# Optimization experiments

Measured on AMD Instinct MI355X. Metric: run time of the kernel, lower is better.

The kernel has to match this reference:

```python
import jax, jax.numpy as jnp
import numpy as np

# ---- static config (severity=3 -> params (0.4, 1, 1)) ----
B, C, H, W = 64, 3, 224, 224
SIGMA = 0.4
MAX_DELTA = 1
ITERATIONS = 1
RADIUS = int(4.0 * SIGMA + 0.5)  # scipy/skimage default truncate=4.0 -> radius 2
_x = np.arange(-RADIUS, RADIUS + 1, dtype=np.float64)
_k = np.exp(-0.5 * (_x / SIGMA) ** 2)
KERNEL = jnp.asarray(_k / _k.sum(), dtype=jnp.float32)  # 5 taps

# swap coordinate order: y = H-1..1 (outer), x = W-1..1 (inner), repeated ITERATIONS times
_ys = np.arange(H - MAX_DELTA, MAX_DELTA - 1, -1, dtype=np.int32)
_xs = np.arange(W - MAX_DELTA, MAX_DELTA - 1, -1, dtype=np.int32)
YS = jnp.asarray(np.tile(np.repeat(_ys, _xs.size), ITERATIONS))  # [ITER*N]
XS = jnp.asarray(np.tile(np.tile(_xs, _ys.size), ITERATIONS))    # [ITER*N]
N_SWAPS = YS.shape[0]


def _gaussian_blur(img):
    """Separable Gaussian, mode='nearest' (edge pad), img [B,H,W,C] float."""
    p = jnp.pad(img, ((0, 0), (RADIUS, RADIUS), (0, 0), (0, 0)), mode='edge')
    img = sum(KERNEL[i] * p[:, i:i + H] for i in range(2 * RADIUS + 1))
    p = jnp.pad(img, ((0, 0), (0, 0), (RADIUS, RADIUS), (0, 0)), mode='edge')
    img = sum(KERNEL[i] * p[:, :, i:i + W] for i in range(2 * RADIUS + 1))
    return img


def _swap_single(img, d):
    """Sequential random pixel swaps. img [H,W,C]; d [N_SWAPS,2] in {-1,0,1}."""
    def body(im, t):
        y, x, dy, dx = t
        yp = jnp.clip(y + dy, 0, H - 1)
        xp = jnp.clip(x + dx, 0, W - 1)
        a = im[y, x]
        b = im[yp, xp]
        # set order matches original temp-swap (self-swap is identity)
        im = im.at[y, x].set(b).at[yp, xp].set(a)
        return im, None
    im, _ = jax.lax.scan(body, img, (YS, XS, d[:, 0], d[:, 1]))
    return im


def setup_inputs() -> dict:
    key = jax.random.key(0)
    k1, k2 = jax.random.split(key)
    x = jax.random.uniform(k1, (B, C, H, W), dtype=jnp.float32)
    deltas = jax.random.randint(k2, (B, N_SWAPS, 2), 0, 3, dtype=jnp.int32)
    return {"x": x, "deltas": deltas}


def reference(x, deltas):
    # tensor_to_numpy_uint8: clamp(x*255) then byte() (truncation)
    img = jnp.floor(jnp.clip(x * 255.0, 0.0, 255.0))        # [B,C,H,W], uint8 values
    img = jnp.transpose(img, (0, 2, 3, 1))                   # [B,H,W,C]
    # first blur + np.uint8 cast (truncation)
    img = jnp.floor(_gaussian_blur(img / 255.0) * 255.0)
    # sequential random pixel swaps, per image
    d = deltas - 1                                           # values in {-1,0,1}
    img = jax.vmap(_swap_single)(img, d)
    # second blur, clip, uint8 cast, then /255 back to float tensor
    img = _gaussian_blur(img / 255.0)
    img = jnp.floor(jnp.clip(img * 255.0, 0.0, 255.0)) / 255.0
    return jnp.transpose(img, (0, 3, 1, 2))                  # [B,C,H,W]
```

## Files before the change

kernel.cpp:

```cpp
#include <hip/hip_runtime.h>
#include <hip/hip_bf16.h>

#define KW0 0.91921792f
#define KW1 0.04038762f
#define KW2 3.42560e-6f

#define HH 224
#define WW 224
#define NSW 49729
#define LEAF_SLOT 676
#define LEAF_IMG 150748
#define P_STRIDE 50176

__global__ __launch_bounds__(256) void build_kernel(const int* __restrict__ deltas,
                                                    unsigned short* __restrict__ leafG) {
    const int j = blockIdx.x;
    const int b = blockIdx.y;
    const int U = j * 32;

    __shared__ __align__(16) unsigned short smA[32 * LEAF_SLOT];
    __shared__ unsigned pk[32 * 29];

    const int tid = threadIdx.x;
    const int u = U + tid;

    {
        const int2* Dbase = (const int2*)deltas + (size_t)b * NSW + (size_t)U * 223;
        for (int w = tid; w < 32 * 28; w += 256) {
            const int r = w / 28, k = w - r * 28;
            if (U + r < 223) {
                const int base = r * 223 + 8 * k;
                unsigned word = 0;
#pragma unroll
                for (int jj = 0; jj < 8; ++jj) {
                    const int i = 8 * k + jj;
                    unsigned idx = 5u;
                    if (i < 223) {
                        int2 d = Dbase[base + jj];
                        unsigned px = (unsigned)d.x, py = (unsigned)d.y;
                        if (U + r == 0) px = min(px, 1u);
                        if (i == 0) py = min(py, 1u);
                        idx = px * 4u + py;
                    }
                    word |= idx << (4 * jj);
                }
                pk[r * 29 + k] = word;
            }
        }
    }
    __syncthreads();

    if (tid < 32 && u < 223) {
        const int y = 223 - u;
        const unsigned b0r = (unsigned)(y - 1) << 8;
        const unsigned b1r = (unsigned)y << 8;
        const unsigned b2r = (unsigned)(y + 1) << 8;
        unsigned short* Lf = &smA[tid * LEAF_SLOT];
        const unsigned* pkr = &pk[tid * 29];

        unsigned w00 = b0r + 222, w01 = b0r + 223, w02 = b0r + 224;
        unsigned w10 = b1r + 222, w11 = b1r + 223, w12 = b1r + 224;
        unsigned w20 = b2r + 222, w21 = b2r + 223, w22 = b2r + 224;

        unsigned wA_ = pkr[0], wB_ = pkr[1], wC_ = pkr[2];

#define GB_STEP(KK, CA, CB, CC) {                                               \
            const int x_ = 223 - (ibase + (KK));                                \
            const unsigned wsel_ = (((KK) >> 3) == 0) ? wA_                     \
                                 : ((((KK) >> 3) == 1) ? wB_ : wC_);            \
            const unsigned idx_ = (wsel_ >> (4 * ((KK) & 7))) & 15u;            \
            const unsigned pr_ = idx_ >> 2, pc_ = idx_ & 3u;                    \
            const bool pc0_ = (pc_ == 0u), pc1_ = (pc_ == 1u);                  \
            const bool pr0_ = (pr_ == 0u), pr1_ = (pr_ == 1u);                  \
            const unsigned s0_ = pc0_ ? w0##CA : (pc1_ ? w0##CB : w0##CC);      \
            const unsigned s1_ = pc0_ ? w1##CA : (pc1_ ? w1##CB : w1##CC);      \
            const unsigned s2_ = pc0_ ? w2##CA : (pc1_ ? w2##CB : w2##CC);      \
            const unsigned v_ = pr0_ ? s0_ : (pr1_ ? s1_ : s2_);                \
            const unsigned c_ = w1##CB;                                         \
            w0##CA = idx_ == 0u  ? c_ : w0##CA;                                 \
            w0##CB = idx_ == 1u  ? c_ : w0##CB;                                 \
            w0##CC = idx_ == 2u  ? c_ : w0##CC;                                 \
            w1##CA = idx_ == 4u  ? c_ : w1##CA;                                 \
            w1##CC = idx_ == 6u  ? c_ : w1##CC;                                 \
            w2##CA = idx_ == 8u  ? c_ : w2##CA;                                 \
            w2##CB = idx_ == 9u  ? c_ : w2##CB;                                 \
            w2##CC = idx_ == 10u ? c_ : w2##CC;                                 \
            w1##CB = v_;                                                        \
            Lf[x_ + 1]   = (unsigned short)w0##CC;                              \
            Lf[x_ + 225] = (unsigned short)w1##CC;                              \
            Lf[x_ + 449] = (unsigned short)w2##CC;                              \
            w0##CC = b0r + (unsigned)(x_ - 2);                                  \
            w1##CC = b1r + (unsigned)(x_ - 2);                                  \
            w2##CC = b2r + (unsigned)(x_ - 2);                                  \
        }
#define GB_TRIPLE(K0) GB_STEP((K0), 0, 1, 2) GB_STEP((K0)+1, 2, 0, 1) GB_STEP((K0)+2, 1, 2, 0)
        for (int blk = 0; blk < 9; ++blk) {
            const int ibase = 24 * blk;
            const unsigned nA_ = pkr[min(3 * blk + 3, 27)];
            const unsigned nB_ = pkr[min(3 * blk + 4, 27)];
            const unsigned nC_ = pkr[min(3 * blk + 5, 27)];
            GB_TRIPLE(0)  GB_TRIPLE(3)  GB_TRIPLE(6)  GB_TRIPLE(9)
            GB_TRIPLE(12) GB_TRIPLE(15) GB_TRIPLE(18) GB_TRIPLE(21)
            wA_ = nA_; wB_ = nB_; wC_ = nC_;
        }
        {
            const int ibase = 216;
            GB_TRIPLE(0) GB_TRIPLE(3) GB_STEP(6, 0, 1, 2)
        }
        Lf[1] = (unsigned short)w01; Lf[225] = (unsigned short)w11; Lf[449] = (unsigned short)w21;
        Lf[0] = (unsigned short)w00; Lf[224] = (unsigned short)w10; Lf[448] = (unsigned short)w20;
#undef GB_TRIPLE
#undef GB_STEP
    }
    __syncthreads();

    const int nuT = min(32, 223 - U);
    uint2* dst = (uint2*)(leafG + (size_t)b * LEAF_IMG + (size_t)U * LEAF_SLOT);
    const uint2* srcp = (const uint2*)smA;
    for (int l = tid; l < nuT * (LEAF_SLOT / 4); l += 256) dst[l] = srcp[l];
}

__global__ __launch_bounds__(256) void chaseP_kernel(const unsigned short* __restrict__ leafG,
                                                     unsigned short* __restrict__ P) {
    const int b = blockIdx.y;
    const int base = blockIdx.x * 2048;
    const unsigned short* L = leafG + (size_t)b * LEAF_IMG;
    unsigned short* Pb = P + (size_t)b * P_STRIDE;
    const int e0 = base + (int)threadIdx.x * 8;
    if (e0 >= P_STRIDE) return;

    unsigned rv[8], cv[8]; bool done[8]; int us[8];
    const int pr0 = e0 / 224, pc0 = e0 - pr0 * 224;
    int umax = -1;
#pragma unroll
    for (int t = 0; t < 8; ++t) {
        const int pc = pc0 + t;
        const int pr = pr0 + (pc >= 224 ? 1 : 0);
        rv[t] = (unsigned)pr;
        cv[t] = (unsigned)(pc >= 224 ? pc - 224 : pc);
        us[t] = min(222, 224 - pr);
        done[t] = false;
        umax = max(umax, us[t]);
    }
    for (int u = umax; u >= 0; --u) {
        const unsigned short* Lu = L + u * LEAF_SLOT;
        const int bot = 222 - u;
        bool all = true;
#pragma unroll
        for (int t = 0; t < 8; ++t) {
            if (!done[t] && u <= us[t]) {
                if ((int)rv[t] < bot) done[t] = true;
                else {
                    const unsigned q = Lu[__mul24((int)rv[t] - bot, 224) + (int)cv[t]];
                    rv[t] = q >> 8;
                    cv[t] = q & 255u;
                }
            }
            all = all && done[t];
        }
        if (all) break;
    }
    unsigned res[8];
#pragma unroll
    for (int t = 0; t < 8; ++t)
        res[t] = (unsigned)(__mul24((int)rv[t], 224) + (int)cv[t]);
    uint4 v;
    v.x = res[0] | (res[1] << 16);
    v.y = res[2] | (res[3] << 16);
    v.z = res[4] | (res[5] << 16);
    v.w = res[6] | (res[7] << 16);
    *(uint4*)(Pb + e0) = v;
}

__global__ __launch_bounds__(256) void blur1_kernel(const float* __restrict__ x,
                                                    unsigned char* __restrict__ img) {
    const int rb = blockIdx.x, c = blockIdx.y, b = blockIdx.z;
    const int y0 = rb * 8;
    __shared__ float A[12][WW];
    __shared__ float Bv[8][WW];
    const float* xp = x + ((size_t)(b * 3 + c)) * HH * WW;

    for (int l = threadIdx.x; l < 12 * 56; l += 256) {
        int r = l / 56, k4 = (l - r * 56) * 4;
        int gy = min(max(y0 + r - 2, 0), HH - 1);
        float4 v = *(const float4*)(xp + gy * WW + k4);
        A[r][k4]     = floorf(fminf(fmaxf(v.x * 255.0f, 0.0f), 255.0f));
        A[r][k4 + 1] = floorf(fminf(fmaxf(v.y * 255.0f, 0.0f), 255.0f));
        A[r][k4 + 2] = floorf(fminf(fmaxf(v.z * 255.0f, 0.0f), 255.0f));
        A[r][k4 + 3] = floorf(fminf(fmaxf(v.w * 255.0f, 0.0f), 255.0f));
    }
    __syncthreads();
    for (int l = threadIdx.x; l < 8 * WW; l += 256) {
        int r = l / WW, xx = l - r * WW;
        Bv[r][xx] = KW2 * A[r][xx] + KW1 * A[r + 1][xx] + KW0 * A[r + 2][xx]
                  + KW1 * A[r + 3][xx] + KW2 * A[r + 4][xx];
    }
    __syncthreads();
    unsigned char* op = img + ((size_t)(b * 3 + c)) * HH * WW;
    for (int l = threadIdx.x; l < 8 * WW; l += 256) {
        int r = l / WW, xx = l - r * WW;
        int c0 = max(xx - 2, 0), c1 = max(xx - 1, 0);
        int c3 = min(xx + 1, WW - 1), c4 = min(xx + 2, WW - 1);
        float s = KW2 * Bv[r][c0] + KW1 * Bv[r][c1] + KW0 * Bv[r][xx]
                + KW1 * Bv[r][c3] + KW2 * Bv[r][c4];
        op[(y0 + r) * WW + xx] = (unsigned char)floorf(s);
    }
}

__global__ __launch_bounds__(256) void blur2_apply_kernel(const unsigned char* __restrict__ img,
                                                          const unsigned short* __restrict__ P,
                                                          float* __restrict__ out) {
    const int rb = blockIdx.x, c = blockIdx.y, b = blockIdx.z;
    const int y0 = rb * 8;
    __shared__ float A[12][WW];
    __shared__ float Bv[8][WW];
    const unsigned char* ip = img + ((size_t)(b * 3 + c)) * HH * WW;
    const unsigned short* Pp = P + (size_t)b * P_STRIDE;

    for (int l = threadIdx.x; l < 12 * 28; l += 256) {
        int r = l / 28, g8 = (l - r * 28) * 8;
        int gy = min(max(y0 + r - 2, 0), HH - 1);
        uint4 pe = *(const uint4*)(Pp + gy * WW + g8);
        A[r][g8]     = (float)ip[pe.x & 0xffffu];
        A[r][g8 + 1] = (float)ip[pe.x >> 16];
        A[r][g8 + 2] = (float)ip[pe.y & 0xffffu];
        A[r][g8 + 3] = (float)ip[pe.y >> 16];
        A[r][g8 + 4] = (float)ip[pe.z & 0xffffu];
        A[r][g8 + 5] = (float)ip[pe.z >> 16];
        A[r][g8 + 6] = (float)ip[pe.w & 0xffffu];
        A[r][g8 + 7] = (float)ip[pe.w >> 16];
    }
    __syncthreads();
    for (int l = threadIdx.x; l < 8 * WW; l += 256) {
        int r = l / WW, xx = l - r * WW;
        Bv[r][xx] = KW2 * A[r][xx] + KW1 * A[r + 1][xx] + KW0 * A[r + 2][xx]
                  + KW1 * A[r + 3][xx] + KW2 * A[r + 4][xx];
    }
    __syncthreads();
    float* op = out + ((size_t)(b * 3 + c)) * HH * WW;
    for (int l = threadIdx.x; l < 8 * WW; l += 256) {
        int r = l / WW, xx = l - r * WW;
        int c0 = max(xx - 2, 0), c1 = max(xx - 1, 0);
        int c3 = min(xx + 1, WW - 1), c4 = min(xx + 2, WW - 1);
        float s = KW2 * Bv[r][c0] + KW1 * Bv[r][c1] + KW0 * Bv[r][xx]
                + KW1 * Bv[r][c3] + KW2 * Bv[r][c4];
        s = fminf(fmaxf(s, 0.0f), 255.0f);
        op[(y0 + r) * WW + xx] = floorf(s) / 255.0f;
    }
}

__global__ __launch_bounds__(256) void apply_kernel(unsigned char* __restrict__ img,
                                                    const unsigned short* __restrict__ P) {
    const int plane = blockIdx.x;
    const int b = plane / 3;
    __shared__ __align__(16) unsigned char im[HH * WW];
    unsigned char* g = img + (size_t)plane * (HH * WW);
    for (int l = threadIdx.x; l < (HH * WW) / 16; l += 256)
        ((int4*)im)[l] = ((const int4*)g)[l];
    __syncthreads();
    const unsigned short* Pp = P + (size_t)b * P_STRIDE;
    for (int t = threadIdx.x; t < (HH * WW) / 8; t += 256) {
        uint4 pe = ((const uint4*)Pp)[t];
        unsigned e0 = pe.x & 0xffffu, e1 = pe.x >> 16;
        unsigned e2 = pe.y & 0xffffu, e3 = pe.y >> 16;
        unsigned e4 = pe.z & 0xffffu, e5 = pe.z >> 16;
        unsigned e6 = pe.w & 0xffffu, e7 = pe.w >> 16;
        unsigned lo = (unsigned)im[e0] | ((unsigned)im[e1] << 8)
                    | ((unsigned)im[e2] << 16) | ((unsigned)im[e3] << 24);
        unsigned hi = (unsigned)im[e4] | ((unsigned)im[e5] << 8)
                    | ((unsigned)im[e6] << 16) | ((unsigned)im[e7] << 24);
        ((uint2*)g)[t] = make_uint2(lo, hi);
    }
}

__global__ __launch_bounds__(256) void blur2_kernel(const unsigned char* __restrict__ img,
                                                    float* __restrict__ out) {
    const int rb = blockIdx.x, c = blockIdx.y, b = blockIdx.z;
    const int y0 = rb * 8;
    __shared__ float A[12][WW];
    __shared__ float Bv[8][WW];
    const unsigned char* ip = img + ((size_t)(b * 3 + c)) * HH * WW;

    for (int l = threadIdx.x; l < 12 * WW; l += 256) {
        int r = l / WW, xx = l - r * WW;
        int gy = min(max(y0 + r - 2, 0), HH - 1);
        A[r][xx] = (float)ip[gy * WW + xx];
    }
    __syncthreads();
    for (int l = threadIdx.x; l < 8 * WW; l += 256) {
        int r = l / WW, xx = l - r * WW;
        Bv[r][xx] = KW2 * A[r][xx] + KW1 * A[r + 1][xx] + KW0 * A[r + 2][xx]
                  + KW1 * A[r + 3][xx] + KW2 * A[r + 4][xx];
    }
    __syncthreads();
    float* op = out + ((size_t)(b * 3 + c)) * HH * WW;
    for (int l = threadIdx.x; l < 8 * WW; l += 256) {
        int r = l / WW, xx = l - r * WW;
        int c0 = max(xx - 2, 0), c1 = max(xx - 1, 0);
        int c3 = min(xx + 1, WW - 1), c4 = min(xx + 2, WW - 1);
        float s = KW2 * Bv[r][c0] + KW1 * Bv[r][c1] + KW0 * Bv[r][xx]
                + KW1 * Bv[r][c3] + KW2 * Bv[r][c4];
        s = fminf(fmaxf(s, 0.0f), 255.0f);
        op[(y0 + r) * WW + xx] = floorf(s) / 255.0f;
    }
}

extern "C" void kernel_launch(void* const* d_in, const int* in_sizes, int n_in,
                              void* d_out, int out_size, void* d_ws, size_t ws_size,
                              hipStream_t stream) {
    const float* x      = (const float*)d_in[0];
    const int*   deltas = (const int*)d_in[1];
    float*       out    = (float*)d_out;
    unsigned char* img  = (unsigned char*)d_ws;

    const size_t imgBytes  = 9633792;
    const size_t leafBytes = (size_t)64 * LEAF_IMG * 2;
    const size_t pBytes    = (size_t)64 * P_STRIDE * 2;
    const bool big_ws = ws_size >= imgBytes + leafBytes + pBytes;

    if (big_ws) {
        unsigned short* leafG = (unsigned short*)(img + imgBytes);
        unsigned short* P     = (unsigned short*)(img + imgBytes + leafBytes);
        build_kernel<<<dim3(7, 64), 256, 0, stream>>>(deltas, leafG);
        chaseP_kernel<<<dim3(25, 64), 256, 0, stream>>>(leafG, P);
        blur1_kernel<<<dim3(28, 3, 64), 256, 0, stream>>>(x, img);
        blur2_apply_kernel<<<dim3(28, 3, 64), 256, 0, stream>>>(img, P, out);
    } else {
        unsigned short* leafG = (unsigned short*)d_out;
        unsigned short* pF    = leafG + (size_t)64 * LEAF_IMG;
        build_kernel<<<dim3(7, 64), 256, 0, stream>>>(deltas, leafG);
        chaseP_kernel<<<dim3(25, 64), 256, 0, stream>>>(leafG, pF);
        blur1_kernel<<<dim3(28, 3, 64), 256, 0, stream>>>(x, img);
        apply_kernel<<<dim3(192), 256, 0, stream>>>(img, pF);
        blur2_kernel<<<dim3(28, 3, 64), 256, 0, stream>>>(img, out);
    }
}
```

Baseline: 109.9 us.

## Fuse leaf build with pointer chase in shared memory, merge blur1 with delta packing

Merges the first blur and the delta packing into one launch, using a block-index split so the two independent jobs share one grid. Replaces the separate build and chase kernels with a single kernel per image half. That kernel builds the swap leaves in shared memory in three row chunks and chases the permutation through them, so the leaf table never round-trips through global memory. The cost is fewer kernel launches and less global traffic. In exchange, the build/chase stage runs on only 128 large blocks, and each chunk's build runs serially on up to 75 threads, which could limit parallelism.

```diff
diff --git a/kernel.cpp b/kernel.cpp
--- a/kernel.cpp
+++ b/kernel.cpp
@@ -8,64 +8,141 @@
 #define HH 224
 #define WW 224
 #define NSW 49729
-#define LEAF_SLOT 676
-#define LEAF_IMG 150748
 #define P_STRIDE 50176
-
-__global__ __launch_bounds__(256) void build_kernel(const int* __restrict__ deltas,
-                                                    unsigned short* __restrict__ leafG) {
-    const int j = blockIdx.x;
-    const int b = blockIdx.y;
-    const int U = j * 32;
-
-    __shared__ __align__(16) unsigned short smA[32 * LEAF_SLOT];
-    __shared__ unsigned pk[32 * 29];
-
+#define LSLOT 672
+
+__global__ __launch_bounds__(256) void prep2_kernel(const float* __restrict__ x,
+                                                    const int* __restrict__ deltas,
+                                                    unsigned char* __restrict__ img,
+                                                    unsigned* __restrict__ pkG) {
+    const int bid = blockIdx.x;
     const int tid = threadIdx.x;
-    const int u = U + tid;
-
-    {
-        const int2* Dbase = (const int2*)deltas + (size_t)b * NSW + (size_t)U * 223;
-        for (int w = tid; w < 32 * 28; w += 256) {
-            const int r = w / 28, k = w - r * 28;
-            if (U + r < 223) {
-                const int base = r * 223 + 8 * k;
-                unsigned word = 0;
+    __shared__ float A[12][WW];
+    __shared__ float Bv[8][WW];
+
+    if (bid < 5376) {
+        const int rb = bid % 28;
+        const int c  = (bid / 28) % 3;
+        const int b  = bid / 84;
+        const int y0 = rb * 8;
+        const float* xp = x + ((size_t)(b * 3 + c)) * HH * WW;
+
+        for (int l = tid; l < 12 * 56; l += 256) {
+            int r = l / 56, k4 = (l - r * 56) * 4;
+            int gy = min(max(y0 + r - 2, 0), HH - 1);
+            float4 v = *(const float4*)(xp + gy * WW + k4);
+            A[r][k4]     = floorf(fminf(fmaxf(v.x * 255.0f, 0.0f), 255.0f));
+            A[r][k4 + 1] = floorf(fminf(fmaxf(v.y * 255.0f, 0.0f), 255.0f));
+            A[r][k4 + 2] = floorf(fminf(fmaxf(v.z * 255.0f, 0.0f), 255.0f));
+            A[r][k4 + 3] = floorf(fminf(fmaxf(v.w * 255.0f, 0.0f), 255.0f));
+        }
+        __syncthreads();
+        for (int l = tid; l < 8 * WW; l += 256) {
+            int r = l / WW, xx = l - r * WW;
+            Bv[r][xx] = KW2 * A[r][xx] + KW1 * A[r + 1][xx] + KW0 * A[r + 2][xx]
+                      + KW1 * A[r + 3][xx] + KW2 * A[r + 4][xx];
+        }
+        __syncthreads();
+        unsigned char* op = img + ((size_t)(b * 3 + c)) * HH * WW;
+        for (int l = tid; l < 8 * WW; l += 256) {
+            int r = l / WW, xx = l - r * WW;
+            int c0 = max(xx - 2, 0), c1 = max(xx - 1, 0);
+            int c3 = min(xx + 1, WW - 1), c4 = min(xx + 2, WW - 1);
+            float s = KW2 * Bv[r][c0] + KW1 * Bv[r][c1] + KW0 * Bv[r][xx]
+                    + KW1 * Bv[r][c3] + KW2 * Bv[r][c4];
+            op[(y0 + r) * WW + xx] = (unsigned char)floorf(s);
+        }
+    } else {
+        const int pidx = (bid - 5376) * 256 + tid;
+        for (int w = pidx; w < 64 * 223 * 29; w += 448 * 256) {
+            const int word = w % 29;
+            const int rowg = w / 29;
+            const int b = rowg / 223, u = rowg - b * 223;
+            const int2* D = (const int2*)deltas + (size_t)b * NSW + (size_t)u * 223;
+            unsigned wordv;
+            if (word < 28) {
+                wordv = 0;
 #pragma unroll
                 for (int jj = 0; jj < 8; ++jj) {
-                    const int i = 8 * k + jj;
+                    const int i = 8 * word + 1 + jj;
                     unsigned idx = 5u;
                     if (i < 223) {
-                        int2 d = Dbase[base + jj];
+                        int2 d = D[i];
                         unsigned px = (unsigned)d.x, py = (unsigned)d.y;
-                        if (U + r == 0) px = min(px, 1u);
-                        if (i == 0) py = min(py, 1u);
+                        if (u == 0) px = min(px, 1u);
                         idx = px * 4u + py;
                     }
-                    word |= idx << (4 * jj);
-                }
-                pk[r * 29 + k] = word;
-            }
-        }
-    }
-    __syncthreads();
-
-    if (tid < 32 && u < 223) {
-        const int y = 223 - u;
-        const unsigned b0r = (unsigned)(y - 1) << 8;
-        const unsigned b1r = (unsigned)y << 8;
-        const unsigned b2r = (unsigned)(y + 1) << 8;
-        unsigned short* Lf = &smA[tid * LEAF_SLOT];
-        const unsigned* pkr = &pk[tid * 29];
-
-        unsigned w00 = b0r + 222, w01 = b0r + 223, w02 = b0r + 224;
-        unsigned w10 = b1r + 222, w11 = b1r + 223, w12 = b1r + 224;
-        unsigned w20 = b2r + 222, w21 = b2r + 223, w22 = b2r + 224;
-
-        unsigned wA_ = pkr[0], wB_ = pkr[1], wC_ = pkr[2];
-
+                    wordv |= idx << (4 * jj);
+                }
+            } else {
+                int2 d = D[0];
+                unsigned px = (unsigned)d.x;
+                unsigned py = min((unsigned)d.y, 1u);
+                if (u == 0) px = min(px, 1u);
+                wordv = px * 4u + py;
+            }
+            pkG[(size_t)rowg * 29 + word] = wordv;
+        }
+    }
+}
+
+__global__ __launch_bounds__(1024) void buildchase_kernel(const unsigned* __restrict__ pkG,
+                                                          unsigned short* __restrict__ P) {
+    const int sp = blockIdx.x;
+    const int b  = blockIdx.y;
+    __shared__ unsigned short leaf[75 * LSLOT];
+    __shared__ unsigned pk[75 * 29];
+    const int tid = threadIdx.x;
+    unsigned short* Pb = P + (size_t)b * P_STRIDE;
+    const unsigned* pkImg = pkG + (size_t)b * 223 * 29;
+
+    for (int ch = 0; ch < 3; ++ch) {
+        const int lo = (ch == 0) ? 148 : ((ch == 1) ? 74 : 0);
+        const int hi = (ch == 0) ? 223 : ((ch == 1) ? 148 : 74);
+        const int nr = hi - lo;
+
+        for (int w = tid; w < nr * 29; w += 1024)
+            pk[w] = pkImg[(size_t)lo * 29 + w];
+        __syncthreads();
+
+        if (tid < nr) {
+            const int u = lo + tid;
+            const int y = 223 - u;
+            const unsigned b0r = (unsigned)(y - 1) << 8;
+            const unsigned b1r = (unsigned)y << 8;
+            const unsigned b2r = (unsigned)(y + 1) << 8;
+            unsigned short* Lf = &leaf[tid * LSLOT];
+            const unsigned* pkr = &pk[tid * 29];
+
+            unsigned w00 = b0r + 222, w01 = b0r + 223, w02 = b0r + 224;
+            unsigned w10 = b1r + 222, w11 = b1r + 223, w12 = b1r + 224;
+            unsigned w20 = b2r + 222, w21 = b2r + 223, w22 = b2r + 224;
+
+            {
+                const unsigned idx_ = pkr[28] & 15u;
+                const unsigned pr_ = idx_ >> 2, pc_ = idx_ & 3u;
+                const bool pc0_ = (pc_ == 0u), pc1_ = (pc_ == 1u);
+                const bool pr0_ = (pr_ == 0u), pr1_ = (pr_ == 1u);
+                const unsigned s0_ = pc0_ ? w00 : (pc1_ ? w01 : w02);
+                const unsigned s1_ = pc0_ ? w10 : (pc1_ ? w11 : w12);
+                const unsigned s2_ = pc0_ ? w20 : (pc1_ ? w21 : w22);
+                const unsigned v_ = pr0_ ? s0_ : (pr1_ ? s1_ : s2_);
+                const unsigned c_ = w11;
+                w00 = idx_ == 0u  ? c_ : w00;
+                w01 = idx_ == 1u  ? c_ : w01;
+                w02 = idx_ == 2u  ? c_ : w02;
+                w10 = idx_ == 4u  ? c_ : w10;
+                w12 = idx_ == 6u  ? c_ : w12;
+                w20 = idx_ == 8u  ? c_ : w20;
+                w21 = idx_ == 9u  ? c_ : w21;
+                w22 = idx_ == 10u ? c_ : w22;
+                w11 = v_;
+                w02 = b0r + 221; w12 = b1r + 221; w22 = b2r + 221;
+            }
+
+            unsigned wA_ = pkr[0], wB_ = pkr[1], wC_ = pkr[2];
 #define GB_STEP(KK, CA, CB, CC) {                                               \
-            const int x_ = 223 - (ibase + (KK));                                \
+            const int x_ = 222 - (jbase + (KK));                                \
             const unsigned wsel_ = (((KK) >> 3) == 0) ? wA_                     \
                                  : ((((KK) >> 3) == 1) ? wB_ : wC_);            \
             const unsigned idx_ = (wsel_ >> (4 * ((KK) & 7))) & 15u;            \
@@ -93,117 +170,87 @@
             w1##CC = b1r + (unsigned)(x_ - 2);                                  \
             w2##CC = b2r + (unsigned)(x_ - 2);                                  \
         }
-#define GB_TRIPLE(K0) GB_STEP((K0), 0, 1, 2) GB_STEP((K0)+1, 2, 0, 1) GB_STEP((K0)+2, 1, 2, 0)
-        for (int blk = 0; blk < 9; ++blk) {
-            const int ibase = 24 * blk;
-            const unsigned nA_ = pkr[min(3 * blk + 3, 27)];
-            const unsigned nB_ = pkr[min(3 * blk + 4, 27)];
-            const unsigned nC_ = pkr[min(3 * blk + 5, 27)];
-            GB_TRIPLE(0)  GB_TRIPLE(3)  GB_TRIPLE(6)  GB_TRIPLE(9)
-            GB_TRIPLE(12) GB_TRIPLE(15) GB_TRIPLE(18) GB_TRIPLE(21)
-            wA_ = nA_; wB_ = nB_; wC_ = nC_;
-        }
-        {
-            const int ibase = 216;
-            GB_TRIPLE(0) GB_TRIPLE(3) GB_STEP(6, 0, 1, 2)
-        }
-        Lf[1] = (unsigned short)w01; Lf[225] = (unsigned short)w11; Lf[449] = (unsigned short)w21;
-        Lf[0] = (unsigned short)w00; Lf[224] = (unsigned short)w10; Lf[448] = (unsigned short)w20;
+#define GB_TRIPLE(K0) GB_STEP((K0), 2, 0, 1) GB_STEP((K0)+1, 1, 2, 0) GB_STEP((K0)+2, 0, 1, 2)
+            for (int blk = 0; blk < 9; ++blk) {
+                const int jbase = 24 * blk;
+                const unsigned nA_ = pkr[min(3 * blk + 3, 27)];
+                const unsigned nB_ = pkr[min(3 * blk + 4, 27)];
+                const unsigned nC_ = pkr[min(3 * blk + 5, 27)];
+                GB_TRIPLE(0)  GB_TRIPLE(3)  GB_TRIPLE(6)  GB_TRIPLE(9)
+                GB_TRIPLE(12) GB_TRIPLE(15) GB_TRIPLE(18) GB_TRIPLE(21)
+                wA_ = nA_; wB_ = nB_; wC_ = nC_;
+            }
+            {
+                const int jbase = 216;
+                GB_TRIPLE(0) GB_TRIPLE(3)
+            }
+            Lf[1] = (unsigned short)w01; Lf[225] = (unsigned short)w11; Lf[449] = (unsigned short)w21;
+            Lf[0] = (unsigned short)w00; Lf[224] = (unsigned short)w10; Lf[448] = (unsigned short)w20;
 #undef GB_TRIPLE
 #undef GB_STEP
-    }
-    __syncthreads();
-
-    const int nuT = min(32, 223 - U);
-    uint2* dst = (uint2*)(leafG + (size_t)b * LEAF_IMG + (size_t)U * LEAF_SLOT);
-    const uint2* srcp = (const uint2*)smA;
-    for (int l = tid; l < nuT * (LEAF_SLOT / 4); l += 256) dst[l] = srcp[l];
-}
-
-__global__ __launch_bounds__(256) void chaseP_kernel(const unsigned short* __restrict__ leafG,
-                                                     unsigned short* __restrict__ P) {
-    const int b = blockIdx.y;
-    const int base = blockIdx.x * 2048;
-    const unsigned short* L = leafG + (size_t)b * LEAF_IMG;
-    unsigned short* Pb = P + (size_t)b * P_STRIDE;
-    const int e0 = base + (int)threadIdx.x * 8;
-    if (e0 >= P_STRIDE) return;
-
-    unsigned rv[8], cv[8]; bool done[8]; int us[8];
-    const int pr0 = e0 / 224, pc0 = e0 - pr0 * 224;
-    int umax = -1;
-#pragma unroll
-    for (int t = 0; t < 8; ++t) {
-        const int pc = pc0 + t;
-        const int pr = pr0 + (pc >= 224 ? 1 : 0);
-        rv[t] = (unsigned)pr;
-        cv[t] = (unsigned)(pc >= 224 ? pc - 224 : pc);
-        us[t] = min(222, 224 - pr);
-        done[t] = false;
-        umax = max(umax, us[t]);
-    }
-    for (int u = umax; u >= 0; --u) {
-        const unsigned short* Lu = L + u * LEAF_SLOT;
-        const int bot = 222 - u;
-        bool all = true;
-#pragma unroll
-        for (int t = 0; t < 8; ++t) {
-            if (!done[t] && u <= us[t]) {
-                if ((int)rv[t] < bot) done[t] = true;
-                else {
-                    const unsigned q = Lu[__mul24((int)rv[t] - bot, 224) + (int)cv[t]];
-                    rv[t] = q >> 8;
-                    cv[t] = q & 255u;
-                }
-            }
-            all = all && done[t];
-        }
-        if (all) break;
-    }
-    unsigned res[8];
-#pragma unroll
-    for (int t = 0; t < 8; ++t)
-        res[t] = (unsigned)(__mul24((int)rv[t], 224) + (int)cv[t]);
-    uint4 v;
-    v.x = res[0] | (res[1] << 16);
-    v.y = res[2] | (res[3] << 16);
-    v.z = res[4] | (res[5] << 16);
-    v.w = res[6] | (res[7] << 16);
-    *(uint4*)(Pb + e0) = v;
-}
-
-__global__ __launch_bounds__(256) void blur1_kernel(const float* __restrict__ x,
-                                                    unsigned char* __restrict__ img) {
-    const int rb = blockIdx.x, c = blockIdx.y, b = blockIdx.z;
-    const int y0 = rb * 8;
-    __shared__ float A[12][WW];
-    __shared__ float Bv[8][WW];
-    const float* xp = x + ((size_t)(b * 3 + c)) * HH * WW;
-
-    for (int l = threadIdx.x; l < 12 * 56; l += 256) {
-        int r = l / 56, k4 = (l - r * 56) * 4;
-        int gy = min(max(y0 + r - 2, 0), HH - 1);
-        float4 v = *(const float4*)(xp + gy * WW + k4);
-        A[r][k4]     = floorf(fminf(fmaxf(v.x * 255.0f, 0.0f), 255.0f));
-        A[r][k4 + 1] = floorf(fminf(fmaxf(v.y * 255.0f, 0.0f), 255.0f));
-        A[r][k4 + 2] = floorf(fminf(fmaxf(v.z * 255.0f, 0.0f), 255.0f));
-        A[r][k4 + 3] = floorf(fminf(fmaxf(v.w * 255.0f, 0.0f), 255.0f));
-    }
-    __syncthreads();
-    for (int l = threadIdx.x; l < 8 * WW; l += 256) {
-        int r = l / WW, xx = l - r * WW;
-        Bv[r][xx] = KW2 * A[r][xx] + KW1 * A[r + 1][xx] + KW0 * A[r + 2][xx]
-                  + KW1 * A[r + 3][xx] + KW2 * A[r + 4][xx];
-    }
-    __syncthreads();
-    unsigned char* op = img + ((size_t)(b * 3 + c)) * HH * WW;
-    for (int l = threadIdx.x; l < 8 * WW; l += 256) {
-        int r = l / WW, xx = l - r * WW;
-        int c0 = max(xx - 2, 0), c1 = max(xx - 1, 0);
-        int c3 = min(xx + 1, WW - 1), c4 = min(xx + 2, WW - 1);
-        float s = KW2 * Bv[r][c0] + KW1 * Bv[r][c1] + KW0 * Bv[r][xx]
-                + KW1 * Bv[r][c3] + KW2 * Bv[r][c4];
-        op[(y0 + r) * WW + xx] = (unsigned char)floorf(s);
+        }
+        __syncthreads();
+
+        const int gBase = sp * 3136;
+        for (int batch = 0; batch < 4; ++batch) {
+            const int g = gBase + batch * 1024 + tid;
+            if (g - gBase < 3136) {
+                unsigned pos[8];
+                if (ch == 0) {
+                    const int e0 = g * 8;
+#pragma unroll
+                    for (int t = 0; t < 8; ++t) {
+                        const int e = e0 + t;
+                        const int rr = e / 224;
+                        pos[t] = ((unsigned)rr << 8) | (unsigned)(e - rr * 224);
+                    }
+                } else {
+                    uint4 v = *(const uint4*)(Pb + g * 8);
+                    pos[0] = v.x & 0xffffu; pos[1] = v.x >> 16;
+                    pos[2] = v.y & 0xffffu; pos[3] = v.y >> 16;
+                    pos[4] = v.z & 0xffffu; pos[5] = v.z >> 16;
+                    pos[6] = v.w & 0xffffu; pos[7] = v.w >> 16;
+                }
+                int uu[8]; bool act[8]; bool live = false;
+#pragma unroll
+                for (int t = 0; t < 8; ++t) {
+                    const int rv = (int)(pos[t] >> 8);
+                    const int us = min(hi - 1, 224 - rv);
+                    act[t] = (us >= lo) && (rv >= 222 - us);
+                    uu[t] = us;
+                    live = live || act[t];
+                }
+                while (__any(live ? 1 : 0)) {
+                    live = false;
+#pragma unroll
+                    for (int t = 0; t < 8; ++t) {
+                        if (act[t]) {
+                            const int bot = 222 - uu[t];
+                            const int off = (int)(pos[t] >> 8) - bot;
+                            const unsigned v = leaf[(uu[t] - lo) * LSLOT + off * 224
+                                                    + (int)(pos[t] & 255u)];
+                            pos[t] = v;
+                            uu[t]--;
+                            act[t] = (uu[t] >= lo) && ((int)(v >> 8) >= 222 - uu[t]);
+                            live = live || act[t];
+                        }
+                    }
+                }
+                if (ch == 2) {
+#pragma unroll
+                    for (int t = 0; t < 8; ++t)
+                        pos[t] = (unsigned)(__mul24((int)(pos[t] >> 8), 224)
+                                            + (int)(pos[t] & 255u));
+                }
+                uint4 o;
+                o.x = pos[0] | (pos[1] << 16);
+                o.y = pos[2] | (pos[3] << 16);
+                o.z = pos[4] | (pos[5] << 16);
+                o.w = pos[6] | (pos[7] << 16);
+                *(uint4*)(Pb + g * 8) = o;
+            }
+        }
+        __syncthreads();
     }
 }
 
@@ -313,25 +360,22 @@
     float*       out    = (float*)d_out;
     unsigned char* img  = (unsigned char*)d_ws;
 
-    const size_t imgBytes  = 9633792;
-    const size_t leafBytes = (size_t)64 * LEAF_IMG * 2;
-    const size_t pBytes    = (size_t)64 * P_STRIDE * 2;
-    const bool big_ws = ws_size >= imgBytes + leafBytes + pBytes;
-
-    if (big_ws) {
-        unsigned short* leafG = (unsigned short*)(img + imgBytes);
-        unsigned short* P     = (unsigned short*)(img + imgBytes + leafBytes);
-        build_kernel<<<dim3(7, 64), 256, 0, stream>>>(deltas, leafG);
-        chaseP_kernel<<<dim3(25, 64), 256, 0, stream>>>(leafG, P);
-        blur1_kernel<<<dim3(28, 3, 64), 256, 0, stream>>>(x, img);
+    const size_t imgBytes = 9633792;
+    const size_t pkBytes  = (size_t)64 * 223 * 29 * 4;
+    const size_t pBytes   = (size_t)64 * P_STRIDE * 2;
+
+    if (ws_size >= imgBytes + pkBytes + pBytes) {
+        unsigned* pkG       = (unsigned*)(img + imgBytes);
+        unsigned short* P   = (unsigned short*)(img + imgBytes + pkBytes);
+        prep2_kernel<<<dim3(5824), 256, 0, stream>>>(x, deltas, img, pkG);
+        buildchase_kernel<<<dim3(2, 64), 1024, 0, stream>>>(pkG, P);
         blur2_apply_kernel<<<dim3(28, 3, 64), 256, 0, stream>>>(img, P, out);
     } else {
-        unsigned short* leafG = (unsigned short*)d_out;
-        unsigned short* pF    = leafG + (size_t)64 * LEAF_IMG;
-        build_kernel<<<dim3(7, 64), 256, 0, stream>>>(deltas, leafG);
-        chaseP_kernel<<<dim3(25, 64), 256, 0, stream>>>(leafG, pF);
-        blur1_kernel<<<dim3(28, 3, 64), 256, 0, stream>>>(x, img);
-        apply_kernel<<<dim3(192), 256, 0, stream>>>(img, pF);
+        unsigned* pkG       = (unsigned*)d_out;
+        unsigned short* P   = (unsigned short*)((char*)d_out + pkBytes);
+        prep2_kernel<<<dim3(5824), 256, 0, stream>>>(x, deltas, img, pkG);
+        buildchase_kernel<<<dim3(2, 64), 1024, 0, stream>>>(pkG, P);
+        apply_kernel<<<dim3(192), 256, 0, stream>>>(img, P);
         blur2_kernel<<<dim3(28, 3, 64), 256, 0, stream>>>(img, out);
     }
 }
```

Result: slower. 198.4 us (+80.6%).

## Merge swap-leaf build and first blur into one heterogeneous prep kernel

Applied to the files above, without the earlier changes.

The build kernel and blur1 kernel become one launch: the first 1792 blocks build leaf tables (8 rows per block instead of 32), and the remaining blocks do the first blur. This removes a kernel launch boundary, and it spreads the serial per-row swap chains over more blocks so they can overlap with the bandwidth-bound blur. The cost is that only 8 of 256 threads do the serial work in build blocks, and the shared-memory union is sized to the larger of the two uses.

```diff
diff --git a/kernel.cpp b/kernel.cpp
--- a/kernel.cpp
+++ b/kernel.cpp
@@ -12,57 +12,61 @@
 #define LEAF_IMG 150748
 #define P_STRIDE 50176
 
-__global__ __launch_bounds__(256) void build_kernel(const int* __restrict__ deltas,
-                                                    unsigned short* __restrict__ leafG) {
-    const int j = blockIdx.x;
-    const int b = blockIdx.y;
-    const int U = j * 32;
-
-    __shared__ __align__(16) unsigned short smA[32 * LEAF_SLOT];
-    __shared__ unsigned pk[32 * 29];
-
+__global__ __launch_bounds__(256) void prep_kernel(const float* __restrict__ x,
+                                                   const int* __restrict__ deltas,
+                                                   unsigned char* __restrict__ img,
+                                                   unsigned short* __restrict__ leafG) {
+    __shared__ __align__(16) unsigned char smem[17920];
+    const int bid = blockIdx.x;
     const int tid = threadIdx.x;
-    const int u = U + tid;
-
-    {
-        const int2* Dbase = (const int2*)deltas + (size_t)b * NSW + (size_t)U * 223;
-        for (int w = tid; w < 32 * 28; w += 256) {
-            const int r = w / 28, k = w - r * 28;
-            if (U + r < 223) {
-                const int base = r * 223 + 8 * k;
-                unsigned word = 0;
+
+    if (bid < 1792) {
+        const int j = bid % 28;
+        const int b = bid / 28;
+        const int U = j * 8;
+        unsigned short* smA = (unsigned short*)smem;
+        unsigned* pk = (unsigned*)(smem + 10816);
+        const int u = U + tid;
+
+        {
+            const int2* Dbase = (const int2*)deltas + (size_t)b * NSW + (size_t)U * 223;
+            for (int w = tid; w < 8 * 28; w += 256) {
+                const int r = w / 28, k = w - r * 28;
+                if (U + r < 223) {
+                    const int base = r * 223 + 8 * k;
+                    unsigned word = 0;
 #pragma unroll
-                for (int jj = 0; jj < 8; ++jj) {
-                    const int i = 8 * k + jj;
-                    unsigned idx = 5u;
-                    if (i < 223) {
-                        int2 d = Dbase[base + jj];
-                        unsigned px = (unsigned)d.x, py = (unsigned)d.y;
-                        if (U + r == 0) px = min(px, 1u);
-                        if (i == 0) py = min(py, 1u);
-                        idx = px * 4u + py;
+                    for (int jj = 0; jj < 8; ++jj) {
+                        const int i = 8 * k + jj;
+                        unsigned idx = 5u;
+                        if (i < 223) {
+                            int2 d = Dbase[base + jj];
+                            unsigned px = (unsigned)d.x, py = (unsigned)d.y;
+                            if (U + r == 0) px = min(px, 1u);
+                            if (i == 0) py = min(py, 1u);
+                            idx = px * 4u + py;
+                        }
+                        word |= idx << (4 * jj);
                     }
-                    word |= idx << (4 * jj);
+                    pk[r * 29 + k] = word;
                 }
-                pk[r * 29 + k] = word;
             }
         }
-    }
-    __syncthreads();
-
-    if (tid < 32 && u < 223) {
-        const int y = 223 - u;
-        const unsigned b0r = (unsigned)(y - 1) << 8;
-        const unsigned b1r = (unsigned)y << 8;
-        const unsigned b2r = (unsigned)(y + 1) << 8;
-        unsigned short* Lf = &smA[tid * LEAF_SLOT];
-        const unsigned* pkr = &pk[tid * 29];
-
-        unsigned w00 = b0r + 222, w01 = b0r + 223, w02 = b0r + 224;
-        unsigned w10 = b1r + 222, w11 = b1r + 223, w12 = b1r + 224;
-        unsigned w20 = b2r + 222, w21 = b2r + 223, w22 = b2r + 224;
-
-        unsigned wA_ = pkr[0], wB_ = pkr[1], wC_ = pkr[2];
+        __syncthreads();
+
+        if (tid < 8 && u < 223) {
+            const int y = 223 - u;
+            const unsigned b0r = (unsigned)(y - 1) << 8;
+            const unsigned b1r = (unsigned)y << 8;
+            const unsigned b2r = (unsigned)(y + 1) << 8;
+            unsigned short* Lf = &smA[tid * LEAF_SLOT];
+            const unsigned* pkr = &pk[tid * 29];
+
+            unsigned w00 = b0r + 222, w01 = b0r + 223, w02 = b0r + 224;
+            unsigned w10 = b1r + 222, w11 = b1r + 223, w12 = b1r + 224;
+            unsigned w20 = b2r + 222, w21 = b2r + 223, w22 = b2r + 224;
+
+            unsigned wA_ = pkr[0], wB_ = pkr[1], wC_ = pkr[2];
 
 #define GB_STEP(KK, CA, CB, CC) {                                               \
             const int x_ = 223 - (ibase + (KK));                                \
@@ -94,30 +98,67 @@
             w2##CC = b2r + (unsigned)(x_ - 2);                                  \
         }
 #define GB_TRIPLE(K0) GB_STEP((K0), 0, 1, 2) GB_STEP((K0)+1, 2, 0, 1) GB_STEP((K0)+2, 1, 2, 0)
-        for (int blk = 0; blk < 9; ++blk) {
-            const int ibase = 24 * blk;
-            const unsigned nA_ = pkr[min(3 * blk + 3, 27)];
-            const unsigned nB_ = pkr[min(3 * blk + 4, 27)];
-            const unsigned nC_ = pkr[min(3 * blk + 5, 27)];
-            GB_TRIPLE(0)  GB_TRIPLE(3)  GB_TRIPLE(6)  GB_TRIPLE(9)
-            GB_TRIPLE(12) GB_TRIPLE(15) GB_TRIPLE(18) GB_TRIPLE(21)
-            wA_ = nA_; wB_ = nB_; wC_ = nC_;
-        }
-        {
-            const int ibase = 216;
-            GB_TRIPLE(0) GB_TRIPLE(3) GB_STEP(6, 0, 1, 2)
-        }
-        Lf[1] = (unsigned short)w01; Lf[225] = (unsigned short)w11; Lf[449] = (unsigned short)w21;
-        Lf[0] = (unsigned short)w00; Lf[224] = (unsigned short)w10; Lf[448] = (unsigned short)w20;
+            for (int blk = 0; blk < 9; ++blk) {
+                const int ibase = 24 * blk;
+                const unsigned nA_ = pk[tid * 29 + min(3 * blk + 3, 27)];
+                const unsigned nB_ = pk[tid * 29 + min(3 * blk + 4, 27)];
+                const unsigned nC_ = pk[tid * 29 + min(3 * blk + 5, 27)];
+                GB_TRIPLE(0)  GB_TRIPLE(3)  GB_TRIPLE(6)  GB_TRIPLE(9)
+                GB_TRIPLE(12) GB_TRIPLE(15) GB_TRIPLE(18) GB_TRIPLE(21)
+                wA_ = nA_; wB_ = nB_; wC_ = nC_;
+            }
+            {
+                const int ibase = 216;
+                GB_TRIPLE(0) GB_TRIPLE(3) GB_STEP(6, 0, 1, 2)
+            }
+            Lf[1] = (unsigned short)w01; Lf[225] = (unsigned short)w11; Lf[449] = (unsigned short)w21;
+            Lf[0] = (unsigned short)w00; Lf[224] = (unsigned short)w10; Lf[448] = (unsigned short)w20;
 #undef GB_TRIPLE
 #undef GB_STEP
-    }
-    __syncthreads();
-
-    const int nuT = min(32, 223 - U);
-    uint2* dst = (uint2*)(leafG + (size_t)b * LEAF_IMG + (size_t)U * LEAF_SLOT);
-    const uint2* srcp = (const uint2*)smA;
-    for (int l = tid; l < nuT * (LEAF_SLOT / 4); l += 256) dst[l] = srcp[l];
+        }
+        __syncthreads();
+
+        const int nuT = min(8, 223 - U);
+        uint2* dst = (uint2*)(leafG + (size_t)b * LEAF_IMG + (size_t)U * LEAF_SLOT);
+        const uint2* srcp = (const uint2*)smA;
+        for (int l = tid; l < nuT * (LEAF_SLOT / 4); l += 256) dst[l] = srcp[l];
+    } else {
+        const int k = bid - 1792;
+        const int rb = k % 28;
+        const int c  = (k / 28) % 3;
+        const int b  = k / 84;
+        const int y0 = rb * 8;
+        float* A  = (float*)smem;
+        float* Bv = A + 12 * WW;
+        const float* xp = x + ((size_t)(b * 3 + c)) * HH * WW;
+
+        for (int l = tid; l < 12 * 56; l += 256) {
+            int r = l / 56, k4 = (l - r * 56) * 4;
+            int gy = min(max(y0 + r - 2, 0), HH - 1);
+            float4 v = *(const float4*)(xp + gy * WW + k4);
+            A[r * WW + k4]     = floorf(fminf(fmaxf(v.x * 255.0f, 0.0f), 255.0f));
+            A[r * WW + k4 + 1] = floorf(fminf(fmaxf(v.y * 255.0f, 0.0f), 255.0f));
+            A[r * WW + k4 + 2] = floorf(fminf(fmaxf(v.z * 255.0f, 0.0f), 255.0f));
+            A[r * WW + k4 + 3] = floorf(fminf(fmaxf(v.w * 255.0f, 0.0f), 255.0f));
+        }
+        __syncthreads();
+        for (int l = tid; l < 8 * WW; l += 256) {
+            int r = l / WW, xx = l - r * WW;
+            Bv[r * WW + xx] = KW2 * A[r * WW + xx] + KW1 * A[(r + 1) * WW + xx]
+                            + KW0 * A[(r + 2) * WW + xx] + KW1 * A[(r + 3) * WW + xx]
+                            + KW2 * A[(r + 4) * WW + xx];
+        }
+        __syncthreads();
+        unsigned char* op = img + ((size_t)(b * 3 + c)) * HH * WW;
+        for (int l = tid; l < 8 * WW; l += 256) {
+            int r = l / WW, xx = l - r * WW;
+            int c0 = max(xx - 2, 0), c1 = max(xx - 1, 0);
+            int c3 = min(xx + 1, WW - 1), c4 = min(xx + 2, WW - 1);
+            float s = KW2 * Bv[r * WW + c0] + KW1 * Bv[r * WW + c1] + KW0 * Bv[r * WW + xx]
+                    + KW1 * Bv[r * WW + c3] + KW2 * Bv[r * WW + c4];
+            op[(y0 + r) * WW + xx] = (unsigned char)floorf(s);
+        }
+    }
 }
 
 __global__ __launch_bounds__(256) void chaseP_kernel(const unsigned short* __restrict__ leafG,
@@ -172,41 +213,6 @@
     *(uint4*)(Pb + e0) = v;
 }
 
-__global__ __launch_bounds__(256) void blur1_kernel(const float* __restrict__ x,
-                                                    unsigned char* __restrict__ img) {
-    const int rb = blockIdx.x, c = blockIdx.y, b = blockIdx.z;
-    const int y0 = rb * 8;
-    __shared__ float A[12][WW];
-    __shared__ float Bv[8][WW];
-    const float* xp = x + ((size_t)(b * 3 + c)) * HH * WW;
-
-    for (int l = threadIdx.x; l < 12 * 56; l += 256) {
-        int r = l / 56, k4 = (l - r * 56) * 4;
-        int gy = min(max(y0 + r - 2, 0), HH - 1);
-        float4 v = *(const float4*)(xp + gy * WW + k4);
-        A[r][k4]     = floorf(fminf(fmaxf(v.x * 255.0f, 0.0f), 255.0f));
-        A[r][k4 + 1] = floorf(fminf(fmaxf(v.y * 255.0f, 0.0f), 255.0f));
-        A[r][k4 + 2] = floorf(fminf(fmaxf(v.z * 255.0f, 0.0f), 255.0f));
-        A[r][k4 + 3] = floorf(fminf(fmaxf(v.w * 255.0f, 0.0f), 255.0f));
-    }
-    __syncthreads();
-    for (int l = threadIdx.x; l < 8 * WW; l += 256) {
-        int r = l / WW, xx = l - r * WW;
-        Bv[r][xx] = KW2 * A[r][xx] + KW1 * A[r + 1][xx] + KW0 * A[r + 2][xx]
-                  + KW1 * A[r + 3][xx] + KW2 * A[r + 4][xx];
-    }
-    __syncthreads();
-    unsigned char* op = img + ((size_t)(b * 3 + c)) * HH * WW;
-    for (int l = threadIdx.x; l < 8 * WW; l += 256) {
-        int r = l / WW, xx = l - r * WW;
-        int c0 = max(xx - 2, 0), c1 = max(xx - 1, 0);
-        int c3 = min(xx + 1, WW - 1), c4 = min(xx + 2, WW - 1);
-        float s = KW2 * Bv[r][c0] + KW1 * Bv[r][c1] + KW0 * Bv[r][xx]
-                + KW1 * Bv[r][c3] + KW2 * Bv[r][c4];
-        op[(y0 + r) * WW + xx] = (unsigned char)floorf(s);
-    }
-}
-
 __global__ __launch_bounds__(256) void blur2_apply_kernel(const unsigned char* __restrict__ img,
                                                           const unsigned short* __restrict__ P,
                                                           float* __restrict__ out) {
@@ -316,21 +322,18 @@
     const size_t imgBytes  = 9633792;
     const size_t leafBytes = (size_t)64 * LEAF_IMG * 2;
     const size_t pBytes    = (size_t)64 * P_STRIDE * 2;
-    const bool big_ws = ws_size >= imgBytes + leafBytes + pBytes;
-
-    if (big_ws) {
+
+    if (ws_size >= imgBytes + leafBytes + pBytes) {
         unsigned short* leafG = (unsigned short*)(img + imgBytes);
         unsigned short* P     = (unsigned short*)(img + imgBytes + leafBytes);
-        build_kernel<<<dim3(7, 64), 256, 0, stream>>>(deltas, leafG);
+        prep_kernel<<<dim3(1792 + 5376), 256, 0, stream>>>(x, deltas, img, leafG);
         chaseP_kernel<<<dim3(25, 64), 256, 0, stream>>>(leafG, P);
-        blur1_kernel<<<dim3(28, 3, 64), 256, 0, stream>>>(x, img);
         blur2_apply_kernel<<<dim3(28, 3, 64), 256, 0, stream>>>(img, P, out);
     } else {
         unsigned short* leafG = (unsigned short*)d_out;
         unsigned short* pF    = leafG + (size_t)64 * LEAF_IMG;
-        build_kernel<<<dim3(7, 64), 256, 0, stream>>>(deltas, leafG);
+        prep_kernel<<<dim3(1792 + 5376), 256, 0, stream>>>(x, deltas, img, leafG);
         chaseP_kernel<<<dim3(25, 64), 256, 0, stream>>>(leafG, pF);
-        blur1_kernel<<<dim3(28, 3, 64), 256, 0, stream>>>(x, img);
         apply_kernel<<<dim3(192), 256, 0, stream>>>(img, pF);
         blur2_kernel<<<dim3(28, 3, 64), 256, 0, stream>>>(img, out);
     }
```

Result: slower. 119.3 us (+8.5%).
